# Optimization experiments

Hardware: AMD Instinct MI355X
Metric: run time of the kernel (lower is better)

Reference implementation:

```python
import jax, jax.numpy as jnp
import numpy as np

TAU = 2.0        # LIF membrane time constant
VTH = 1.0        # spike threshold
VRESET = 0.0     # hard reset voltage
ALPHA = 2.0      # ATan surrogate alpha
LN_EPS = 1e-5


@jax.custom_vjp
def atan_spike(x):
    # Heaviside forward, ATan surrogate backward (spikingjelly surrogate.ATan)
    return (x >= 0.0).astype(x.dtype)

def _atan_fwd(x):
    return atan_spike(x), x

def _atan_bwd(x, g):
    z = (jnp.pi / 2.0) * ALPHA * x
    return (g * (ALPHA / 2.0) / (1.0 + z * z),)

atan_spike.defvjp(_atan_fwd, _atan_bwd)


def layer_norm(x, w, b):
    mu = jnp.mean(x, axis=-1, keepdims=True)
    var = jnp.mean(jnp.square(x - mu), axis=-1, keepdims=True)
    return (x - mu) * jax.lax.rsqrt(var + LN_EPS) * w + b


def time_shift(x):
    # x: [B,T,C] -> x shifted by one step in time, zero-padded at t=0
    return jnp.pad(x, ((0, 0), (1, 0), (0, 0)))[:, :-1]


def wkv(time_decay, time_first, k, v):
    # Numerically-stable RWKV WKV recurrence. k, v: [B,T,C]
    w = -jnp.exp(time_decay)  # [C]
    u = time_first            # [C]
    B, T, C = k.shape
    kT = jnp.moveaxis(k, 1, 0)  # [T,B,C]
    vT = jnp.moveaxis(v, 1, 0)
    init = (jnp.zeros((B, C), k.dtype),
            jnp.zeros((B, C), k.dtype),
            jnp.full((B, C), -1e38, k.dtype))

    def step(carry, kv_t):
        aa, bb, pp = carry
        kt, vt = kv_t
        ww = u + kt
        p = jnp.maximum(pp, ww)
        e1 = jnp.exp(pp - p)
        e2 = jnp.exp(ww - p)
        y = (e1 * aa + e2 * vt) / (e1 * bb + e2)
        ww2 = pp + w
        p2 = jnp.maximum(ww2, kt)
        e1b = jnp.exp(ww2 - p2)
        e2b = jnp.exp(kt - p2)
        return (e1b * aa + e2b * vt, e1b * bb + e2b, p2), y

    _, yT = jax.lax.scan(step, init, (kT, vT))
    return jnp.moveaxis(yT, 0, 1)  # [B,T,C]


def lif(x):
    # MultiStepLIFNode: tau=2, decay_input=True, v_th=1, hard reset to 0.
    # Recurrence runs over the sequence dim (permute(1,0,2) in torch is layout only).
    xT = jnp.moveaxis(x, 1, 0)  # [T,B,C]
    v0 = jnp.zeros_like(xT[0])

    def step(v, xt):
        v = v + (xt - (v - VRESET)) / TAU
        s = atan_spike(v - VTH)
        v = (1.0 - s) * v + s * VRESET
        return v, s

    _, sT = jax.lax.scan(step, v0, xT)
    return jnp.moveaxis(sT, 0, 1)


def rwkv_time_mix(x, time_decay, time_first, mix_k, mix_v, mix_r, Wk, Wv, Wr, Wo):
    xx = time_shift(x)
    xk = x * mix_k + xx * (1.0 - mix_k)
    xv = x * mix_v + xx * (1.0 - mix_v)
    xr = x * mix_r + xx * (1.0 - mix_r)
    k = jnp.einsum('btc,cd->btd', xk, Wk)
    v = jnp.einsum('btc,cd->btd', xv, Wv)
    r = jax.nn.sigmoid(jnp.einsum('btc,cd->btd', xr, Wr))
    y = wkv(time_decay, time_first, k, v)
    return jnp.einsum('btc,cd->btd', r * y, Wo)


def rwkv_channel_mix(x, mix_k, mix_r, Wk, Wv, Wr):
    xx = time_shift(x)
    xk = x * mix_k + xx * (1.0 - mix_k)
    xr = x * mix_r + xx * (1.0 - mix_r)
    k = jnp.square(jax.nn.relu(jnp.einsum('btc,ch->bth', xk, Wk)))  # relu^2
    kv = jnp.einsum('bth,hc->btc', k, Wv)
    return jax.nn.sigmoid(jnp.einsum('btc,cd->btd', xr, Wr)) * kv


def setup_inputs() -> dict:
    key = jax.random.key(0)
    B, T, C, H = 8, 2048, 768, 3072
    ks = jax.random.split(key, 20)
    p = lambda k, shape, s=0.02: (jax.random.normal(k, shape, jnp.float32) * s)
    u = lambda k, shape: jax.random.uniform(k, shape, jnp.float32)
    return {
        'x': jax.random.normal(ks[0], (B, T, C), jnp.float32),
        'ln1_w': jnp.ones((C,), jnp.float32), 'ln1_b': jnp.zeros((C,), jnp.float32),
        'ln2_w': jnp.ones((C,), jnp.float32), 'ln2_b': jnp.zeros((C,), jnp.float32),
        'att_time_decay': p(ks[1], (C,), 1.0),
        'att_time_first': p(ks[2], (C,), 1.0),
        'att_mix_k': u(ks[3], (C,)), 'att_mix_v': u(ks[4], (C,)), 'att_mix_r': u(ks[5], (C,)),
        'att_Wk': p(ks[6], (C, C)), 'att_Wv': p(ks[7], (C, C)),
        'att_Wr': p(ks[8], (C, C)), 'att_Wo': p(ks[9], (C, C)),
        'ffn_mix_k': u(ks[10], (C,)), 'ffn_mix_r': u(ks[11], (C,)),
        'ffn_Wk': p(ks[12], (C, H)), 'ffn_Wv': p(ks[13], (H, C)), 'ffn_Wr': p(ks[14], (C, C)),
    }


def reference(x, ln1_w, ln1_b, ln2_w, ln2_b,
              att_time_decay, att_time_first, att_mix_k, att_mix_v, att_mix_r,
              att_Wk, att_Wv, att_Wr, att_Wo,
              ffn_mix_k, ffn_mix_r, ffn_Wk, ffn_Wv, ffn_Wr):
    # Block.forward with layer_id != 0 (no ln0, att path); dropout in eval mode.
    a = rwkv_time_mix(layer_norm(x, ln1_w, ln1_b), att_time_decay, att_time_first,
                      att_mix_k, att_mix_v, att_mix_r, att_Wk, att_Wv, att_Wr, att_Wo)
    x = x + lif(a)
    f = rwkv_channel_mix(layer_norm(x, ln2_w, ln2_b), ffn_mix_k, ffn_mix_r,
                         ffn_Wk, ffn_Wv, ffn_Wr)
    x = x + lif(f)
    return x
```

## Files before the change

kernel.cpp:

```cpp
#include <hip/hip_runtime.h>

#define B_ 8
#define T_ 2048
#define C_ 768
#define H_ 3072
#define BT_ (B_ * T_)
#define BC_ (B_ * C_)
#define WSEG 128
#define NWSEG 16
#define LSEG 128
#define NLSEG 16
#define LWARM 96

typedef unsigned short u16;
typedef short bf16x8 __attribute__((ext_vector_type(8)));
typedef float f32x4 __attribute__((ext_vector_type(4)));

__device__ __forceinline__ float b2f(u16 u) {
    union { unsigned i; float f; } w; w.i = ((unsigned)u) << 16; return w.f;
}
__device__ __forceinline__ u16 f2b(float f) {
    union { float f; unsigned i; } w; w.f = f;
    return (u16)((w.i + 0x7fffu + ((w.i >> 16) & 1u)) >> 16);
}

typedef __attribute__((address_space(3))) unsigned int lds_u32;
typedef const __attribute__((address_space(1))) unsigned int glb_u32;
__device__ __forceinline__ void gld_lds16(const void* g, void* l) {
    __builtin_amdgcn_global_load_lds((glb_u32*)g, (lds_u32*)l, 16, 0, 0);
}

template<int NOUT>
__global__ void lnmix(const float* __restrict__ x, const float* __restrict__ w,
                      const float* __restrict__ b,
                      const float* __restrict__ m1, const float* __restrict__ m2,
                      const float* __restrict__ m3,
                      u16* __restrict__ o1, u16* __restrict__ o2, u16* __restrict__ o3) {
    int row = blockIdx.x;
    int t = row % T_;
    const float* xr = x + (size_t)row * C_;
    const float* xp = xr - C_;
    int tid = threadIdx.x;
    float s = 0.f, s2 = 0.f, ps = 0.f, ps2 = 0.f;
    for (int i = tid; i < C_; i += 256) {
        float v = xr[i]; s += v; s2 += v * v;
        if (t > 0) { float u = xp[i]; ps += u; ps2 += u * u; }
    }
    for (int off = 32; off > 0; off >>= 1) {
        s += __shfl_down(s, off);  s2 += __shfl_down(s2, off);
        ps += __shfl_down(ps, off); ps2 += __shfl_down(ps2, off);
    }
    __shared__ float red[4][4];
    int wid = tid >> 6, lane = tid & 63;
    if (lane == 0) { red[wid][0] = s; red[wid][1] = s2; red[wid][2] = ps; red[wid][3] = ps2; }
    __syncthreads();
    if (tid == 0) {
        float a0 = 0, a1 = 0, a2 = 0, a3 = 0;
        for (int i = 0; i < 4; ++i) { a0 += red[i][0]; a1 += red[i][1]; a2 += red[i][2]; a3 += red[i][3]; }
        red[0][0] = a0; red[0][1] = a1; red[0][2] = a2; red[0][3] = a3;
    }
    __syncthreads();
    float mu = red[0][0] * (1.f / C_);
    float rs = rsqrtf(red[0][1] * (1.f / C_) - mu * mu + 1e-5f);
    float pmu = red[0][2] * (1.f / C_);
    float prs = rsqrtf(red[0][3] * (1.f / C_) - pmu * pmu + 1e-5f);
    size_t ob = (size_t)row * C_;
    for (int i = tid; i < C_; i += 256) {
        float wi = w[i], bi = b[i];
        float n = (xr[i] - mu) * rs * wi + bi;
        float np = (t > 0) ? (xp[i] - pmu) * prs * wi + bi : 0.f;
        o1[ob + i] = f2b(fmaf(m1[i], n - np, np));
        o2[ob + i] = f2b(fmaf(m2[i], n - np, np));
        if constexpr (NOUT == 3) o3[ob + i] = f2b(fmaf(m3[i], n - np, np));
    }
}

__global__ void tcast(const float* __restrict__ src, u16* __restrict__ dst, int R, int Ncol) {
    __shared__ float t[32][33];
    int c0 = blockIdx.x * 32, r0 = blockIdx.y * 32;
    int col = threadIdx.x & 31, rw = threadIdx.x >> 5;
#pragma unroll
    for (int i = 0; i < 4; ++i) {
        int r = rw + i * 8;
        t[r][col] = src[(size_t)(r0 + r) * Ncol + c0 + col];
    }
    __syncthreads();
#pragma unroll
    for (int i = 0; i < 4; ++i) {
        int r = rw + i * 8;
        dst[(size_t)(c0 + r) * R + r0 + col] = f2b(t[col][r]);
    }
}

__device__ __forceinline__ void gemm_core(const u16* __restrict__ A,
                                          const u16* __restrict__ WT,
                                          int K, int m0, int n0,
                                          u16* As, u16* Bs, f32x4 acc[4][4]) {
    const int tid = threadIdx.x;
    const int lane = tid & 63, wid = tid >> 6;
    const int wr = wid >> 1, wc = wid & 1;
    const int r16 = lane & 15, g = lane >> 4;

    const int srow = tid >> 2;
    const int sslot = tid & 3;
    const int sx = (srow >> 1) & 3;
    const u16* gA0 = A + (size_t)(m0 + srow) * K + ((sslot ^ sx) << 3);
    const u16* gA1 = gA0 + (size_t)64 * K;
    const u16* gB0 = WT + (size_t)(n0 + srow) * K + ((sslot ^ sx) << 3);
    const u16* gB1 = gB0 + (size_t)64 * K;
    u16* lA0 = As + tid * 8;
    u16* lA1 = As + 2048 + tid * 8;
    u16* lB0 = Bs + tid * 8;
    u16* lB1 = Bs + 2048 + tid * 8;

    int offA[4], offB[4];
#pragma unroll
    for (int m = 0; m < 4; ++m) {
        int row = wr * 64 + m * 16 + r16;
        offA[m] = row * 32 + (g ^ ((row >> 1) & 3)) * 8;
        int rob = wc * 64 + m * 16 + r16;
        offB[m] = rob * 32 + (g ^ ((rob >> 1) & 3)) * 8;
    }

    gld_lds16(gA0, lA0); gld_lds16(gA1, lA1);
    gld_lds16(gB0, lB0); gld_lds16(gB1, lB1);
    gA0 += 32; gA1 += 32; gB0 += 32; gB1 += 32;
    __syncthreads();

    const int nk = K >> 5;
    int cur = 0;
    for (int kt = 0; kt < nk; ++kt) {
        const int nxt = cur ^ 1;
        if (kt + 1 < nk) {
            gld_lds16(gA0, lA0 + nxt * 4096);
            gld_lds16(gA1, lA1 + nxt * 4096);
            gld_lds16(gB0, lB0 + nxt * 4096);
            gld_lds16(gB1, lB1 + nxt * 4096);
            gA0 += 32; gA1 += 32; gB0 += 32; gB1 += 32;
        }
        const u16* Ab = As + cur * 4096;
        const u16* Bb = Bs + cur * 4096;
        bf16x8 af[4], bg[4];
#pragma unroll
        for (int m = 0; m < 4; ++m) af[m] = *(const bf16x8*)(Ab + offA[m]);
#pragma unroll
        for (int n = 0; n < 4; ++n) bg[n] = *(const bf16x8*)(Bb + offB[n]);
#pragma unroll
        for (int m = 0; m < 4; ++m)
#pragma unroll
            for (int n = 0; n < 4; ++n)
                acc[m][n] = __builtin_amdgcn_mfma_f32_16x16x32_bf16(af[m], bg[n], acc[m][n], 0, 0, 0);
        __syncthreads();
        cur = nxt;
    }
}

__device__ __forceinline__ void xcd_remap(int& m0, int& n0) {
    const int gx = gridDim.x;
    const int nwg = gx * gridDim.y;
    const int lin = blockIdx.y * gx + blockIdx.x;
    const int q = nwg >> 3, r = nwg & 7;
    const int xcd = lin & 7, pos = lin >> 3;
    const int nid = (xcd < r ? xcd * (q + 1) : r * (q + 1) + (xcd - r) * q) + pos;
    m0 = (nid / gx) << 7;
    n0 = (nid % gx) << 7;
}

template<int MODE, bool OBF, bool EMUL>
__global__ __launch_bounds__(256)
void gemm2(const u16* __restrict__ A, const u16* __restrict__ WT,
           void* __restrict__ Cout, const u16* __restrict__ Emul, int N, int K) {
    __shared__ u16 As[8192];
    __shared__ u16 Bs[8192];
    int m0, n0;
    xcd_remap(m0, n0);
    f32x4 acc[4][4];
#pragma unroll
    for (int i = 0; i < 4; ++i)
#pragma unroll
        for (int j = 0; j < 4; ++j)
#pragma unroll
            for (int q = 0; q < 4; ++q) acc[i][j][q] = 0.f;
    gemm_core(A, WT, K, m0, n0, As, Bs, acc);

    const int lane = threadIdx.x & 63, wid = threadIdx.x >> 6;
    const int wr = wid >> 1, wc = wid & 1;
    const int r16 = lane & 15, g = lane >> 4;
#pragma unroll
    for (int m = 0; m < 4; ++m)
#pragma unroll
        for (int n = 0; n < 4; ++n)
#pragma unroll
            for (int j = 0; j < 4; ++j) {
                int row = m0 + wr * 64 + m * 16 + g * 4 + j;
                int col = n0 + wc * 64 + n * 16 + r16;
                float v = acc[m][n][j];
                if constexpr (MODE == 1) v = 1.f / (1.f + expf(-v));
                if constexpr (MODE == 2) { v = fmaxf(v, 0.f); v = v * v; }
                size_t o = (size_t)row * N + col;
                if constexpr (EMUL) v *= b2f(Emul[o]);
                if constexpr (OBF) ((u16*)Cout)[o] = f2b(v);
                else ((float*)Cout)[o] = v;
            }
}

struct P3 {
    const u16 *A0, *A1, *A2;
    const u16 *W0, *W1, *W2;
    u16 *O0, *O1, *O2;
};
__global__ __launch_bounds__(256)
void proj3(P3 p, int N, int K) {
    __shared__ u16 As[8192];
    __shared__ u16 Bs[8192];
    const int z = blockIdx.z;
    const u16* A = (z == 0) ? p.A0 : (z == 1) ? p.A1 : p.A2;
    const u16* W = (z == 0) ? p.W0 : (z == 1) ? p.W1 : p.W2;
    u16* O = (z == 0) ? p.O0 : (z == 1) ? p.O1 : p.O2;
    int m0, n0;
    xcd_remap(m0, n0);
    f32x4 acc[4][4];
#pragma unroll
    for (int i = 0; i < 4; ++i)
#pragma unroll
        for (int j = 0; j < 4; ++j)
#pragma unroll
            for (int q = 0; q < 4; ++q) acc[i][j][q] = 0.f;
    gemm_core(A, W, K, m0, n0, As, Bs, acc);

    const int lane = threadIdx.x & 63, wid = threadIdx.x >> 6;
    const int wr = wid >> 1, wc = wid & 1;
    const int r16 = lane & 15, g = lane >> 4;
    const bool sig = (z == 2);
#pragma unroll
    for (int m = 0; m < 4; ++m)
#pragma unroll
        for (int n = 0; n < 4; ++n)
#pragma unroll
            for (int j = 0; j < 4; ++j) {
                int row = m0 + wr * 64 + m * 16 + g * 4 + j;
                int col = n0 + wc * 64 + n * 16 + r16;
                float v = acc[m][n][j];
                if (sig) v = 1.f / (1.f + expf(-v));
                O[(size_t)row * N + col] = f2b(v);
            }
}

__global__ void wkv_p1(const float* __restrict__ td, const u16* __restrict__ K,
                       const u16* __restrict__ V, float* __restrict__ st) {
    int bc = blockIdx.x * 256 + threadIdx.x;
    int seg = blockIdx.y;
    int b = bc / C_, c = bc - b * C_;
    float w = -expf(td[c]);
    size_t off = (size_t)b * T_ * C_ + (size_t)seg * WSEG * C_ + c;
    float aa = 0.f, bb = 0.f, pp = -1e38f;
#pragma unroll 4
    for (int i = 0; i < WSEG; ++i) {
        float kt = b2f(K[off + (size_t)i * C_]);
        float vt = b2f(V[off + (size_t)i * C_]);
        float ww2 = pp + w;
        float p2 = fmaxf(ww2, kt);
        float e1 = expf(ww2 - p2);
        float e2 = expf(kt - p2);
        aa = e1 * aa + e2 * vt;
        bb = e1 * bb + e2;
        pp = p2;
    }
    int sidx = seg * 3 * BC_ + bc;
    st[sidx] = aa; st[sidx + BC_] = bb; st[sidx + 2 * BC_] = pp;
}

__global__ void wkv_p2(const float* __restrict__ td, const float* __restrict__ st,
                       float* __restrict__ ini) {
    int bc = blockIdx.x * 256 + threadIdx.x;
    int c = bc % C_;
    float wL = -expf(td[c]) * (float)WSEG;
    float aa = 0.f, bb = 0.f, pp = -1e38f;
    for (int s = 0; s < NWSEG; ++s) {
        int sidx = s * 3 * BC_ + bc;
        ini[sidx] = aa; ini[sidx + BC_] = bb; ini[sidx + 2 * BC_] = pp;
        float la = st[sidx], lb = st[sidx + BC_], lp = st[sidx + 2 * BC_];
        float ppw = pp + wL;
        float p = fmaxf(ppw, lp);
        float e1 = expf(ppw - p), e2 = expf(lp - p);
        aa = e1 * aa + e2 * la;
        bb = e1 * bb + e2 * lb;
        pp = p;
    }
}

__global__ void wkv_p3(const float* __restrict__ td, const float* __restrict__ tf,
                       const u16* __restrict__ K, const u16* __restrict__ V,
                       const u16* __restrict__ R, const float* __restrict__ ini,
                       u16* __restrict__ RY) {
    int bc = blockIdx.x * 256 + threadIdx.x;
    int seg = blockIdx.y;
    int b = bc / C_, c = bc - b * C_;
    float w = -expf(td[c]);
    float u = tf[c];
    int sidx = seg * 3 * BC_ + bc;
    float aa = ini[sidx], bb = ini[sidx + BC_], pp = ini[sidx + 2 * BC_];
    size_t off = (size_t)b * T_ * C_ + (size_t)seg * WSEG * C_ + c;
#pragma unroll 4
    for (int i = 0; i < WSEG; ++i) {
        float kt = b2f(K[off + (size_t)i * C_]);
        float vt = b2f(V[off + (size_t)i * C_]);
        float rr = b2f(R[off + (size_t)i * C_]);
        float ww = u + kt;
        float p = fmaxf(pp, ww);
        float e1 = expf(pp - p);
        float e2 = expf(ww - p);
        RY[off + (size_t)i * C_] = f2b(rr * (e1 * aa + e2 * vt) / (e1 * bb + e2));
        float ww2 = pp + w;
        float p2 = fmaxf(ww2, kt);
        float e1b = expf(ww2 - p2);
        float e2b = expf(kt - p2);
        aa = e1b * aa + e2b * vt;
        bb = e1b * bb + e2b;
        pp = p2;
    }
}

__global__ void lif_add(const float* __restrict__ cur, const float* __restrict__ base,
                        float* __restrict__ out) {
    int bc = blockIdx.x * 256 + threadIdx.x;
    int seg = blockIdx.y;
    int b = bc / C_, c = bc - b * C_;
    size_t rowbase = (size_t)b * T_ * C_ + c;
    int t0 = seg * LSEG;
    int tw = t0 - LWARM; if (tw < 0) tw = 0;
    int nw = t0 - tw;
    float v = 0.f;
    const float* cp = cur + rowbase + (size_t)tw * C_;
#pragma unroll 8
    for (int i = 0; i < nw; ++i) {
        float xt = cp[(size_t)i * C_];
        v += (xt - v) * 0.5f;
        v = (v >= 1.f) ? 0.f : v;
    }
    const float* c2 = cur + rowbase + (size_t)t0 * C_;
    const float* bp = base + rowbase + (size_t)t0 * C_;
    float* op = out + rowbase + (size_t)t0 * C_;
#pragma unroll 8
    for (int i = 0; i < LSEG; ++i) {
        float xt = c2[(size_t)i * C_];
        v += (xt - v) * 0.5f;
        float sp = (v >= 1.f) ? 1.f : 0.f;
        op[(size_t)i * C_] = bp[(size_t)i * C_] + sp;
        v = (sp > 0.f) ? 0.f : v;
    }
}

extern "C" void kernel_launch(void* const* d_in, const int* in_sizes, int n_in,
                              void* d_out, int out_size, void* d_ws, size_t ws_size,
                              hipStream_t stream) {
    const float* x    = (const float*)d_in[0];
    const float* ln1w = (const float*)d_in[1];
    const float* ln1b = (const float*)d_in[2];
    const float* ln2w = (const float*)d_in[3];
    const float* ln2b = (const float*)d_in[4];
    const float* td   = (const float*)d_in[5];
    const float* tf   = (const float*)d_in[6];
    const float* amk  = (const float*)d_in[7];
    const float* amv  = (const float*)d_in[8];
    const float* amr  = (const float*)d_in[9];
    const float* aWk  = (const float*)d_in[10];
    const float* aWv  = (const float*)d_in[11];
    const float* aWr  = (const float*)d_in[12];
    const float* aWo  = (const float*)d_in[13];
    const float* fmk  = (const float*)d_in[14];
    const float* fmr  = (const float*)d_in[15];
    const float* fWk  = (const float*)d_in[16];
    const float* fWv  = (const float*)d_in[17];
    const float* fWr  = (const float*)d_in[18];
    float* out = (float*)d_out;

    const size_t NBC = (size_t)BT_ * C_;
    u16* WkT = (u16*)d_ws;
    u16* WvT = WkT + 589824;
    u16* WrT = WvT + 589824;
    u16* WoT = WrT + 589824;
    u16* FrT = WoT + 589824;
    u16* FkT = FrT + 589824;
    u16* FvT = FkT + 2359296;
    float* st  = (float*)(FvT + 2359296);
    float* ini = st + NWSEG * 3 * BC_;
    u16* S0 = (u16*)(ini + NWSEG * 3 * BC_);
    u16* S1 = S0 + NBC;
    u16* S2 = S1 + NBC;
    u16* S3 = S2 + NBC;
    char* tail = (char*)(S3 + NBC);
    size_t used_fixed = (size_t)((char*)tail - (char*)d_ws);

    int NCH = 4;
    {
        size_t need2 = used_fixed - NBC * 2 + (size_t)(BT_ / 2) * H_ * 2 + (size_t)(BT_ / 2) * C_ * 4;
        if (ws_size >= need2) NCH = 2;
    }
    const int CH = BT_ / NCH;
    u16* Hbuf = S3;
    float* Fbuf = (float*)(S3 + (size_t)CH * H_);

    u16* Kb = (u16*)d_out;
    u16* Vb = Kb + NBC;

    tcast<<<dim3(24, 24), 256, 0, stream>>>(aWk, WkT, 768, 768);
    tcast<<<dim3(24, 24), 256, 0, stream>>>(aWv, WvT, 768, 768);
    tcast<<<dim3(24, 24), 256, 0, stream>>>(aWr, WrT, 768, 768);
    tcast<<<dim3(24, 24), 256, 0, stream>>>(aWo, WoT, 768, 768);
    tcast<<<dim3(24, 24), 256, 0, stream>>>(fWr, FrT, 768, 768);
    tcast<<<dim3(96, 24), 256, 0, stream>>>(fWk, FkT, 768, 3072);
    tcast<<<dim3(24, 96), 256, 0, stream>>>(fWv, FvT, 3072, 768);

    lnmix<3><<<BT_, 256, 0, stream>>>(x, ln1w, ln1b, amk, amv, amr, S0, S1, S2);
    {
        P3 p{S0, S1, S2, WkT, WvT, WrT, Kb, Vb, S3};
        proj3<<<dim3(6, 128, 3), 256, 0, stream>>>(p, C_, C_);
    }
    wkv_p1<<<dim3(BC_ / 256, NWSEG), 256, 0, stream>>>(td, Kb, Vb, st);
    wkv_p2<<<BC_ / 256, 256, 0, stream>>>(td, st, ini);
    wkv_p3<<<dim3(BC_ / 256, NWSEG), 256, 0, stream>>>(td, tf, Kb, Vb, S3, ini, S0);
    float* Af = (float*)S2;
    dim3 gP(6, 128);
    gemm2<0, false, false><<<gP, 256, 0, stream>>>(S0, WoT, Af, nullptr, C_, C_);
    lif_add<<<dim3(BC_ / 256, NLSEG), 256, 0, stream>>>(Af, x, out);
    lnmix<2><<<BT_, 256, 0, stream>>>(out, ln2w, ln2b, fmk, fmr, nullptr, S0, S1, nullptr);
    gemm2<1, true, false><<<gP, 256, 0, stream>>>(S1, FrT, S2, nullptr, C_, C_);
    for (int ch = 0; ch < NCH; ++ch) {
        const u16* xk2c = S0 + (size_t)ch * CH * C_;
        const u16* rrc  = S2 + (size_t)ch * CH * C_;
        dim3 g1(H_ / 128, CH / 128);
        gemm2<2, true, false><<<g1, 256, 0, stream>>>(xk2c, FkT, Hbuf, nullptr, H_, C_);
        dim3 g2(6, CH / 128);
        gemm2<0, false, true><<<g2, 256, 0, stream>>>(Hbuf, FvT, Fbuf, rrc, C_, H_);
        lif_add<<<dim3((CH / T_) * C_ / 256, NLSEG), 256, 0, stream>>>(
            Fbuf, out + (size_t)ch * CH * C_, out + (size_t)ch * CH * C_);
    }
}
```

Before: 617.0 us.

## Widen GEMM tiles to 128x256, store bf16 intermediates, batch weight casts, fewer FFN chunks

```diff
diff --git a/kernel.cpp b/kernel.cpp
--- a/kernel.cpp
+++ b/kernel.cpp
@@ -75,27 +75,36 @@
     }
 }
 
-__global__ void tcast(const float* __restrict__ src, u16* __restrict__ dst, int R, int Ncol) {
+struct TCJ { const float* s; u16* d; int R, Ncol, nbx, b0; };
+struct TC7 { TCJ j[7]; };
+__global__ void tcast_all(TC7 jobs) {
     __shared__ float t[32][33];
-    int c0 = blockIdx.x * 32, r0 = blockIdx.y * 32;
+    int bid = blockIdx.x;
+    int ji = 0;
+#pragma unroll
+    for (int k = 1; k < 7; ++k) if (bid >= jobs.j[k].b0) ji = k;
+    TCJ jb = jobs.j[ji];
+    int local = bid - jb.b0;
+    int bx = local % jb.nbx, by = local / jb.nbx;
+    int c0 = bx * 32, r0 = by * 32;
     int col = threadIdx.x & 31, rw = threadIdx.x >> 5;
 #pragma unroll
     for (int i = 0; i < 4; ++i) {
         int r = rw + i * 8;
-        t[r][col] = src[(size_t)(r0 + r) * Ncol + c0 + col];
+        t[r][col] = jb.s[(size_t)(r0 + r) * jb.Ncol + c0 + col];
     }
     __syncthreads();
 #pragma unroll
     for (int i = 0; i < 4; ++i) {
         int r = rw + i * 8;
-        dst[(size_t)(c0 + r) * R + r0 + col] = f2b(t[col][r]);
+        jb.d[(size_t)(c0 + r) * jb.R + r0 + col] = f2b(t[col][r]);
     }
 }
 
 __device__ __forceinline__ void gemm_core(const u16* __restrict__ A,
                                           const u16* __restrict__ WT,
                                           int K, int m0, int n0,
-                                          u16* As, u16* Bs, f32x4 acc[4][4]) {
+                                          u16* As, u16* Bs, f32x4 acc[4][8]) {
     const int tid = threadIdx.x;
     const int lane = tid & 63, wid = tid >> 6;
     const int wr = wid >> 1, wc = wid & 1;
@@ -108,23 +117,27 @@
     const u16* gA1 = gA0 + (size_t)64 * K;
     const u16* gB0 = WT + (size_t)(n0 + srow) * K + ((sslot ^ sx) << 3);
     const u16* gB1 = gB0 + (size_t)64 * K;
-    u16* lA0 = As + tid * 8;
-    u16* lA1 = As + 2048 + tid * 8;
-    u16* lB0 = Bs + tid * 8;
-    u16* lB1 = Bs + 2048 + tid * 8;
-
-    int offA[4], offB[4];
+    const u16* gB2 = gB0 + (size_t)128 * K;
+    const u16* gB3 = gB0 + (size_t)192 * K;
+    u16* lA = As + tid * 8;
+    u16* lB = Bs + tid * 8;
+
+    int offA[4], offB[8];
 #pragma unroll
     for (int m = 0; m < 4; ++m) {
         int row = wr * 64 + m * 16 + r16;
         offA[m] = row * 32 + (g ^ ((row >> 1) & 3)) * 8;
-        int rob = wc * 64 + m * 16 + r16;
-        offB[m] = rob * 32 + (g ^ ((rob >> 1) & 3)) * 8;
-    }
-
-    gld_lds16(gA0, lA0); gld_lds16(gA1, lA1);
-    gld_lds16(gB0, lB0); gld_lds16(gB1, lB1);
-    gA0 += 32; gA1 += 32; gB0 += 32; gB1 += 32;
+    }
+#pragma unroll
+    for (int n = 0; n < 8; ++n) {
+        int rob = wc * 128 + n * 16 + r16;
+        offB[n] = rob * 32 + (g ^ ((rob >> 1) & 3)) * 8;
+    }
+
+    gld_lds16(gA0, lA);        gld_lds16(gA1, lA + 2048);
+    gld_lds16(gB0, lB);        gld_lds16(gB1, lB + 2048);
+    gld_lds16(gB2, lB + 4096); gld_lds16(gB3, lB + 6144);
+    gA0 += 32; gA1 += 32; gB0 += 32; gB1 += 32; gB2 += 32; gB3 += 32;
     __syncthreads();
 
     const int nk = K >> 5;
@@ -132,23 +145,24 @@
     for (int kt = 0; kt < nk; ++kt) {
         const int nxt = cur ^ 1;
         if (kt + 1 < nk) {
-            gld_lds16(gA0, lA0 + nxt * 4096);
-            gld_lds16(gA1, lA1 + nxt * 4096);
-            gld_lds16(gB0, lB0 + nxt * 4096);
-            gld_lds16(gB1, lB1 + nxt * 4096);
-            gA0 += 32; gA1 += 32; gB0 += 32; gB1 += 32;
+            u16* pA = lA + nxt * 4096;
+            u16* pB = lB + nxt * 8192;
+            gld_lds16(gA0, pA);        gld_lds16(gA1, pA + 2048);
+            gld_lds16(gB0, pB);        gld_lds16(gB1, pB + 2048);
+            gld_lds16(gB2, pB + 4096); gld_lds16(gB3, pB + 6144);
+            gA0 += 32; gA1 += 32; gB0 += 32; gB1 += 32; gB2 += 32; gB3 += 32;
         }
         const u16* Ab = As + cur * 4096;
-        const u16* Bb = Bs + cur * 4096;
-        bf16x8 af[4], bg[4];
+        const u16* Bb = Bs + cur * 8192;
+        bf16x8 af[4], bg[8];
 #pragma unroll
         for (int m = 0; m < 4; ++m) af[m] = *(const bf16x8*)(Ab + offA[m]);
 #pragma unroll
-        for (int n = 0; n < 4; ++n) bg[n] = *(const bf16x8*)(Bb + offB[n]);
+        for (int n = 0; n < 8; ++n) bg[n] = *(const bf16x8*)(Bb + offB[n]);
 #pragma unroll
         for (int m = 0; m < 4; ++m)
 #pragma unroll
-            for (int n = 0; n < 4; ++n)
+            for (int n = 0; n < 8; ++n)
                 acc[m][n] = __builtin_amdgcn_mfma_f32_16x16x32_bf16(af[m], bg[n], acc[m][n], 0, 0, 0);
         __syncthreads();
         cur = nxt;
@@ -163,22 +177,22 @@
     const int xcd = lin & 7, pos = lin >> 3;
     const int nid = (xcd < r ? xcd * (q + 1) : r * (q + 1) + (xcd - r) * q) + pos;
     m0 = (nid / gx) << 7;
-    n0 = (nid % gx) << 7;
-}
-
-template<int MODE, bool OBF, bool EMUL>
-__global__ __launch_bounds__(256)
+    n0 = (nid % gx) << 8;
+}
+
+template<int MODE, bool EMUL>
+__global__ __launch_bounds__(256, 2)
 void gemm2(const u16* __restrict__ A, const u16* __restrict__ WT,
-           void* __restrict__ Cout, const u16* __restrict__ Emul, int N, int K) {
+           u16* __restrict__ Cout, const u16* __restrict__ Emul, int N, int K) {
     __shared__ u16 As[8192];
-    __shared__ u16 Bs[8192];
+    __shared__ u16 Bs[16384];
     int m0, n0;
     xcd_remap(m0, n0);
-    f32x4 acc[4][4];
+    f32x4 acc[4][8];
 #pragma unroll
     for (int i = 0; i < 4; ++i)
 #pragma unroll
-        for (int j = 0; j < 4; ++j)
+        for (int j = 0; j < 8; ++j)
 #pragma unroll
             for (int q = 0; q < 4; ++q) acc[i][j][q] = 0.f;
     gemm_core(A, WT, K, m0, n0, As, Bs, acc);
@@ -189,18 +203,17 @@
 #pragma unroll
     for (int m = 0; m < 4; ++m)
 #pragma unroll
-        for (int n = 0; n < 4; ++n)
+        for (int n = 0; n < 8; ++n)
 #pragma unroll
             for (int j = 0; j < 4; ++j) {
                 int row = m0 + wr * 64 + m * 16 + g * 4 + j;
-                int col = n0 + wc * 64 + n * 16 + r16;
+                int col = n0 + wc * 128 + n * 16 + r16;
                 float v = acc[m][n][j];
                 if constexpr (MODE == 1) v = 1.f / (1.f + expf(-v));
                 if constexpr (MODE == 2) { v = fmaxf(v, 0.f); v = v * v; }
                 size_t o = (size_t)row * N + col;
                 if constexpr (EMUL) v *= b2f(Emul[o]);
-                if constexpr (OBF) ((u16*)Cout)[o] = f2b(v);
-                else ((float*)Cout)[o] = v;
+                Cout[o] = f2b(v);
             }
 }
 
@@ -209,21 +222,21 @@
     const u16 *W0, *W1, *W2;
     u16 *O0, *O1, *O2;
 };
-__global__ __launch_bounds__(256)
+__global__ __launch_bounds__(256, 2)
 void proj3(P3 p, int N, int K) {
     __shared__ u16 As[8192];
-    __shared__ u16 Bs[8192];
+    __shared__ u16 Bs[16384];
     const int z = blockIdx.z;
     const u16* A = (z == 0) ? p.A0 : (z == 1) ? p.A1 : p.A2;
     const u16* W = (z == 0) ? p.W0 : (z == 1) ? p.W1 : p.W2;
     u16* O = (z == 0) ? p.O0 : (z == 1) ? p.O1 : p.O2;
     int m0, n0;
     xcd_remap(m0, n0);
-    f32x4 acc[4][4];
+    f32x4 acc[4][8];
 #pragma unroll
     for (int i = 0; i < 4; ++i)
 #pragma unroll
-        for (int j = 0; j < 4; ++j)
+        for (int j = 0; j < 8; ++j)
 #pragma unroll
             for (int q = 0; q < 4; ++q) acc[i][j][q] = 0.f;
     gemm_core(A, W, K, m0, n0, As, Bs, acc);
@@ -235,11 +248,11 @@
 #pragma unroll
     for (int m = 0; m < 4; ++m)
 #pragma unroll
-        for (int n = 0; n < 4; ++n)
+        for (int n = 0; n < 8; ++n)
 #pragma unroll
             for (int j = 0; j < 4; ++j) {
                 int row = m0 + wr * 64 + m * 16 + g * 4 + j;
-                int col = n0 + wc * 64 + n * 16 + r16;
+                int col = n0 + wc * 128 + n * 16 + r16;
                 float v = acc[m][n][j];
                 if (sig) v = 1.f / (1.f + expf(-v));
                 O[(size_t)row * N + col] = f2b(v);
@@ -321,8 +334,8 @@
     }
 }
 
-__global__ void lif_add(const float* __restrict__ cur, const float* __restrict__ base,
-                        float* __restrict__ out) {
+__global__ void lif_add_b(const u16* __restrict__ cur, const float* __restrict__ base,
+                          float* __restrict__ out) {
     int bc = blockIdx.x * 256 + threadIdx.x;
     int seg = blockIdx.y;
     int b = bc / C_, c = bc - b * C_;
@@ -331,19 +344,19 @@
     int tw = t0 - LWARM; if (tw < 0) tw = 0;
     int nw = t0 - tw;
     float v = 0.f;
-    const float* cp = cur + rowbase + (size_t)tw * C_;
+    const u16* cp = cur + rowbase + (size_t)tw * C_;
 #pragma unroll 8
     for (int i = 0; i < nw; ++i) {
-        float xt = cp[(size_t)i * C_];
+        float xt = b2f(cp[(size_t)i * C_]);
         v += (xt - v) * 0.5f;
         v = (v >= 1.f) ? 0.f : v;
     }
-    const float* c2 = cur + rowbase + (size_t)t0 * C_;
+    const u16* c2 = cur + rowbase + (size_t)t0 * C_;
     const float* bp = base + rowbase + (size_t)t0 * C_;
     float* op = out + rowbase + (size_t)t0 * C_;
 #pragma unroll 8
     for (int i = 0; i < LSEG; ++i) {
-        float xt = c2[(size_t)i * C_];
+        float xt = b2f(c2[(size_t)i * C_]);
         v += (xt - v) * 0.5f;
         float sp = (v >= 1.f) ? 1.f : 0.f;
         op[(size_t)i * C_] = bp[(size_t)i * C_] + sp;
@@ -389,51 +402,52 @@
     u16* S1 = S0 + NBC;
     u16* S2 = S1 + NBC;
     u16* S3 = S2 + NBC;
-    char* tail = (char*)(S3 + NBC);
-    size_t used_fixed = (size_t)((char*)tail - (char*)d_ws);
+    u16* Hbuf = S3 + NBC;
+    size_t fixed_b = (size_t)((char*)Hbuf - (char*)d_ws);
 
     int NCH = 4;
-    {
-        size_t need2 = used_fixed - NBC * 2 + (size_t)(BT_ / 2) * H_ * 2 + (size_t)(BT_ / 2) * C_ * 4;
-        if (ws_size >= need2) NCH = 2;
-    }
+    if (ws_size >= fixed_b + ((size_t)BT_ * H_ + NBC) * 2) NCH = 1;
+    else if (ws_size >= fixed_b + ((size_t)(BT_ / 2) * H_ + NBC / 2) * 2) NCH = 2;
     const int CH = BT_ / NCH;
-    u16* Hbuf = S3;
-    float* Fbuf = (float*)(S3 + (size_t)CH * H_);
+    u16* Fbuf = Hbuf + (size_t)CH * H_;
 
     u16* Kb = (u16*)d_out;
     u16* Vb = Kb + NBC;
 
-    tcast<<<dim3(24, 24), 256, 0, stream>>>(aWk, WkT, 768, 768);
-    tcast<<<dim3(24, 24), 256, 0, stream>>>(aWv, WvT, 768, 768);
-    tcast<<<dim3(24, 24), 256, 0, stream>>>(aWr, WrT, 768, 768);
-    tcast<<<dim3(24, 24), 256, 0, stream>>>(aWo, WoT, 768, 768);
-    tcast<<<dim3(24, 24), 256, 0, stream>>>(fWr, FrT, 768, 768);
-    tcast<<<dim3(96, 24), 256, 0, stream>>>(fWk, FkT, 768, 3072);
-    tcast<<<dim3(24, 96), 256, 0, stream>>>(fWv, FvT, 3072, 768);
+    {
+        TC7 jobs;
+        const float* srcs[7] = {aWk, aWv, aWr, aWo, fWr, fWk, fWv};
+        u16* dsts[7] = {WkT, WvT, WrT, WoT, FrT, FkT, FvT};
+        int Rs[7]    = {768, 768, 768, 768, 768, 768, 3072};
+        int Ns[7]    = {768, 768, 768, 768, 768, 3072, 768};
+        int b0 = 0;
+        for (int k = 0; k < 7; ++k) {
+            jobs.j[k].s = srcs[k]; jobs.j[k].d = dsts[k];
+            jobs.j[k].R = Rs[k]; jobs.j[k].Ncol = Ns[k];
+            jobs.j[k].nbx = Ns[k] / 32; jobs.j[k].b0 = b0;
+            b0 += (Ns[k] / 32) * (Rs[k] / 32);
+        }
+        tcast_all<<<b0, 256, 0, stream>>>(jobs);
+    }
 
     lnmix<3><<<BT_, 256, 0, stream>>>(x, ln1w, ln1b, amk, amv, amr, S0, S1, S2);
     {
         P3 p{S0, S1, S2, WkT, WvT, WrT, Kb, Vb, S3};
-        proj3<<<dim3(6, 128, 3), 256, 0, stream>>>(p, C_, C_);
+        proj3<<<dim3(3, 128, 3), 256, 0, stream>>>(p, C_, C_);
     }
     wkv_p1<<<dim3(BC_ / 256, NWSEG), 256, 0, stream>>>(td, Kb, Vb, st);
     wkv_p2<<<BC_ / 256, 256, 0, stream>>>(td, st, ini);
     wkv_p3<<<dim3(BC_ / 256, NWSEG), 256, 0, stream>>>(td, tf, Kb, Vb, S3, ini, S0);
-    float* Af = (float*)S2;
-    dim3 gP(6, 128);
-    gemm2<0, false, false><<<gP, 256, 0, stream>>>(S0, WoT, Af, nullptr, C_, C_);
-    lif_add<<<dim3(BC_ / 256, NLSEG), 256, 0, stream>>>(Af, x, out);
+    gemm2<0, false><<<dim3(3, 128), 256, 0, stream>>>(S0, WoT, S1, nullptr, C_, C_);
+    lif_add_b<<<dim3(BC_ / 256, NLSEG), 256, 0, stream>>>(S1, x, out);
     lnmix<2><<<BT_, 256, 0, stream>>>(out, ln2w, ln2b, fmk, fmr, nullptr, S0, S1, nullptr);
-    gemm2<1, true, false><<<gP, 256, 0, stream>>>(S1, FrT, S2, nullptr, C_, C_);
+    gemm2<1, false><<<dim3(3, 128), 256, 0, stream>>>(S1, FrT, S2, nullptr, C_, C_);
     for (int ch = 0; ch < NCH; ++ch) {
         const u16* xk2c = S0 + (size_t)ch * CH * C_;
         const u16* rrc  = S2 + (size_t)ch * CH * C_;
-        dim3 g1(H_ / 128, CH / 128);
-        gemm2<2, true, false><<<g1, 256, 0, stream>>>(xk2c, FkT, Hbuf, nullptr, H_, C_);
-        dim3 g2(6, CH / 128);
-        gemm2<0, false, true><<<g2, 256, 0, stream>>>(Hbuf, FvT, Fbuf, rrc, C_, H_);
-        lif_add<<<dim3((CH / T_) * C_ / 256, NLSEG), 256, 0, stream>>>(
+        gemm2<2, false><<<dim3(12, CH / 128), 256, 0, stream>>>(xk2c, FkT, Hbuf, nullptr, H_, C_);
+        gemm2<0, true><<<dim3(3, CH / 128), 256, 0, stream>>>(Hbuf, FvT, Fbuf, rrc, C_, H_);
+        lif_add_b<<<dim3((CH / T_) * C_ / 256, NLSEG), 256, 0, stream>>>(
             Fbuf, out + (size_t)ch * CH * C_, out + (size_t)ch * CH * C_);
     }
 }
```

Result: faster. 592.9 us (-3.9%).
